# Optimization experiments

Measured on AMD Instinct MI355X. Metric: run time of the kernel, lower is better.

## Reference

```python
import jax, jax.numpy as jnp
import numpy as np

SIZE = 384  # output resolution
SCALE = (0.8, 1.0)


def _bilinear_crop_resize(img, cs, top, left):
    """img: [C,H,W]; cs/top/left: int32 scalars. Crop [top:top+cs, left:left+cs],
    resize to SIZE x SIZE with bilinear, align_corners=False (PyTorch semantics)."""
    csf = cs.astype(jnp.float32)
    # source coords within the crop, clamped like PyTorch (src = max(src,0), upper bounded)
    coords = (jnp.arange(SIZE, dtype=jnp.float32) + 0.5) * (csf / SIZE) - 0.5
    coords = jnp.clip(coords, 0.0, csf - 1.0)
    i0 = jnp.floor(coords).astype(jnp.int32)
    i1 = jnp.minimum(i0 + 1, cs - 1)
    w = coords - i0.astype(jnp.float32)  # [SIZE]
    y0, y1 = i0 + top, i1 + top
    x0, x1 = i0 + left, i1 + left
    wy, wx = w[:, None], w[None, :]
    g = lambda yy, xx: img[:, yy[:, None], xx[None, :]]  # [C,SIZE,SIZE]
    return (g(y0, x0) * (1 - wy) * (1 - wx)
            + g(y0, x1) * (1 - wy) * wx
            + g(y1, x0) * wy * (1 - wx)
            + g(y1, x1) * wy * wx)


def _nearest_crop_resize(msk, cs, top, left):
    """msk: [1,H,W]. PyTorch mode='nearest': src_idx = floor(dst * in/out)."""
    idx = jnp.floor(jnp.arange(SIZE, dtype=jnp.float32) * cs.astype(jnp.float32) / SIZE).astype(jnp.int32)
    idx = jnp.minimum(idx, cs - 1)
    y, x = idx + top, idx + left
    return msk[:, y[:, None], x[None, :]]


def setup_inputs() -> dict:
    key = jax.random.key(0)
    k1, k2, k3, k4, k5 = jax.random.split(key, 5)
    B, C, H, W = 32, 3, 512, 512
    image = jax.random.normal(k1, (B, C, H, W), dtype=jnp.float32)
    mask = (jax.random.uniform(k2, (B, 1, H, W)) > 0.5).astype(jnp.float32)
    scale = jax.random.uniform(k3, (B,), minval=SCALE[0], maxval=SCALE[1])
    crop_size = (scale * min(H, W)).astype(jnp.int32)
    max_y = (H - crop_size).astype(jnp.float32)
    max_x = (W - crop_size).astype(jnp.float32)
    top = jnp.where(max_y > 0, jnp.floor(jax.random.uniform(k4, (B,)) * max_y), 0.0).astype(jnp.int32)
    left = jnp.where(max_x > 0, jnp.floor(jax.random.uniform(k5, (B,)) * max_x), 0.0).astype(jnp.int32)
    return {"image": image, "mask": mask, "crop_size": crop_size, "top": top, "left": left}


def reference(image, mask, crop_size, top, left):
    img_out = jax.vmap(_bilinear_crop_resize)(image, crop_size, top, left)
    msk_out = jax.vmap(_nearest_crop_resize)(mask, crop_size, top, left)
    return img_out, msk_out
```

## Files before the change

### kernel.cpp

```cpp
#include <hip/hip_runtime.h>


constexpr int OUT = 384;
constexpr int H = 512;
constexpr int W = 512;
constexpr int B = 32;
constexpr int C = 3;
constexpr int RPB = 4;
constexpr int GPB = OUT / RPB;
constexpr int NBLK = B * GPB;
constexpr int BPX  = NBLK / 8;
constexpr int NSLOT = 6;
constexpr int LROWS = C * NSLOT;
constexpr int BUFSZ = LROWS * W;

typedef float f32x4 __attribute__((ext_vector_type(4)));

__global__ __launch_bounds__(OUT) void rrc_pair_kernel(
    const float* __restrict__ image,
    const float* __restrict__ mask,
    const int* __restrict__ crop_size,
    const int* __restrict__ top,
    const int* __restrict__ left,
    float* __restrict__ img_out,
    float* __restrict__ msk_out)
{
    __shared__ float lds[BUFSZ + 8];

    const int hw = blockIdx.x;
    const int logical = (hw & 7) * BPX + (hw >> 3);
    const int b  = logical / GPB;
    const int i0 = (logical % GPB) * RPB;
    const int tid = (int)threadIdx.x;

    const int cs = crop_size[b];
    const int t  = top[b];
    const int l  = left[b];
    const float csf = (float)cs;
    const float s   = csf / (float)OUT;

    float cy0 = ((float)i0 + 0.5f) * s - 0.5f;
    cy0 = fminf(fmaxf(cy0, 0.0f), csf - 1.0f);
    const int base_y = (int)floorf(cy0);

    const float* imgb = image + (size_t)b * C * H * W;

    #pragma unroll
    for (int k = 0; k < 6; ++k) {
        const int q   = tid + k * OUT;
        const int r   = q >> 7;
        const int col = (q & 127) * 4;
        const int c    = r / NSLOT;
        const int slot = r % NSLOT;
        const int y = min(t + base_y + slot, H - 1);
        const float* src = imgb + ((size_t)c * H + (size_t)y) * W + col;
        __builtin_amdgcn_global_load_lds(
            (const __attribute__((address_space(1))) void*)src,
            (__attribute__((address_space(3))) void*)&lds[q * 4],
            16, 0, 0);
    }
    if (tid < 8) lds[BUFSZ + tid] = 0.0f;

    float cx = ((float)tid + 0.5f) * s - 0.5f;
    cx = fminf(fmaxf(cx, 0.0f), csf - 1.0f);
    const int   ix0 = (int)floorf(cx);
    const float wx  = cx - (float)ix0;
    const int   x0  = ix0 + l;

    const int mx = min((tid * cs) / OUT, cs - 1) + l;

    float mval[RPB];
    #pragma unroll
    for (int r4 = 0; r4 < RPB; ++r4) {
        const int i = i0 + r4;
        int my = min((i * cs) / OUT, cs - 1);
        mval[r4] = mask[((size_t)b * H + (size_t)(my + t)) * W + mx];
    }

    __syncthreads();

    #pragma unroll
    for (int r4 = 0; r4 < RPB; ++r4) {
        const int i = i0 + r4;
        float cy = ((float)i + 0.5f) * s - 0.5f;
        cy = fminf(fmaxf(cy, 0.0f), csf - 1.0f);
        int   iy0 = (int)floorf(cy);
        int   iy1 = min(iy0 + 1, cs - 1);
        float wy  = cy - (float)iy0;
        const int slot0 = iy0 - base_y;
        const int slot1 = min(iy1 - base_y, NSLOT - 1);

        const float w00 = (1.0f - wy) * (1.0f - wx);
        const float w01 = (1.0f - wy) * wx;
        const float w10 = wy * (1.0f - wx);
        const float w11 = wy * wx;

        const size_t o_base = (size_t)b * C * OUT * OUT + (size_t)i * OUT + (size_t)tid;

        #pragma unroll
        for (int c = 0; c < C; ++c) {
            const float* rA = &lds[(c * NSLOT + slot0) * W + x0];
            const float* rB = &lds[(c * NSLOT + slot1) * W + x0];
            float v00 = rA[0], v01 = rA[1];
            float v10 = rB[0], v11 = rB[1];
            float rr = v00 * w00 + v01 * w01 + v10 * w10 + v11 * w11;
            __builtin_nontemporal_store(rr, img_out + o_base + (size_t)c * OUT * OUT);
        }
        __builtin_nontemporal_store(mval[r4],
            msk_out + (size_t)b * OUT * OUT + (size_t)i * OUT + (size_t)tid);
    }
}

extern "C" void kernel_launch(void* const* d_in, const int* in_sizes, int n_in,
                              void* d_out, int out_size, void* d_ws, size_t ws_size,
                              hipStream_t stream) {
    const float* image = (const float*)d_in[0];
    const float* mask  = (const float*)d_in[1];
    const int* cs      = (const int*)d_in[2];
    const int* top     = (const int*)d_in[3];
    const int* left    = (const int*)d_in[4];

    float* img_out = (float*)d_out;
    float* msk_out = img_out + (size_t)B * C * OUT * OUT;

    dim3 block(OUT);
    dim3 grid(NBLK);
    hipLaunchKernelGGL(rrc_pair_kernel, grid, block, 0, stream,
                       image, mask, cs, top, left, img_out, msk_out);
}
```

Baseline: 33.14 us.

## Split output rows into column stripes and stage only needed source columns in LDS

Each block now handles a 128-wide column stripe of 4 output rows instead of full 384-wide rows, so the grid is three times larger with 128-thread blocks. Only a 176-float-wide window of each source row, aligned to 4 floats, is loaded into LDS rather than the full 512-float row. This cuts wasted global loads of columns the block never reads and lowers LDS per block, which allows more blocks per CU. In exchange, blocks are smaller, per-block setup is repeated more often, and neighbouring stripes load overlapping columns.

```diff
diff --git a/kernel.cpp b/kernel.cpp
--- a/kernel.cpp
+++ b/kernel.cpp
@@ -8,15 +8,19 @@
 constexpr int C = 3;
 constexpr int RPB = 4;
 constexpr int GPB = OUT / RPB;
-constexpr int NBLK = B * GPB;
-constexpr int BPX  = NBLK / 8;
+constexpr int SW  = 128;
+constexpr int NSTRIPE = OUT / SW;
 constexpr int NSLOT = 6;
 constexpr int LROWS = C * NSLOT;
-constexpr int BUFSZ = LROWS * W;
+constexpr int NW  = 176;
+constexpr int NCH = NW / 4;
+constexpr int TOT_CHUNK = LROWS * NCH;
+constexpr int NBLK = B * GPB * NSTRIPE;
+constexpr int BPX  = NBLK / 8;
 
 typedef float f32x4 __attribute__((ext_vector_type(4)));
 
-__global__ __launch_bounds__(OUT) void rrc_pair_kernel(
+__global__ __launch_bounds__(128, 6) void rrc_pair_kernel(
     const float* __restrict__ image,
     const float* __restrict__ mask,
     const int* __restrict__ crop_size,
@@ -25,13 +29,18 @@
     float* __restrict__ img_out,
     float* __restrict__ msk_out)
 {
-    __shared__ float lds[BUFSZ + 8];
+    __shared__ float lds[LROWS * NW + 8];
 
     const int hw = blockIdx.x;
     const int logical = (hw & 7) * BPX + (hw >> 3);
-    const int b  = logical / GPB;
-    const int i0 = (logical % GPB) * RPB;
+    const int b   = logical / (GPB * NSTRIPE);
+    const int rem = logical % (GPB * NSTRIPE);
+    const int grp = rem / NSTRIPE;
+    const int st  = rem % NSTRIPE;
+    const int i0  = grp * RPB;
+    const int c0  = st * SW;
     const int tid = (int)threadIdx.x;
+    const int j   = c0 + tid;
 
     const int cs = crop_size[b];
     const int t  = top[b];
@@ -43,37 +52,43 @@
     cy0 = fminf(fmaxf(cy0, 0.0f), csf - 1.0f);
     const int base_y = (int)floorf(cy0);
 
+    float cx0 = ((float)c0 + 0.5f) * s - 0.5f;
+    cx0 = fminf(fmaxf(cx0, 0.0f), csf - 1.0f);
+    const int gx0 = (int)floorf(cx0);
+    const int cbg = min(l + gx0, W - NW) & ~3;
+
     const float* imgb = image + (size_t)b * C * H * W;
 
     #pragma unroll
-    for (int k = 0; k < 6; ++k) {
-        const int q   = tid + k * OUT;
-        const int r   = q >> 7;
-        const int col = (q & 127) * 4;
-        const int c    = r / NSLOT;
-        const int slot = r % NSLOT;
-        const int y = min(t + base_y + slot, H - 1);
-        const float* src = imgb + ((size_t)c * H + (size_t)y) * W + col;
-        __builtin_amdgcn_global_load_lds(
-            (const __attribute__((address_space(1))) void*)src,
-            (__attribute__((address_space(3))) void*)&lds[q * 4],
-            16, 0, 0);
+    for (int rd = 0; rd < 7; ++rd) {
+        const int q = rd * 128 + tid;
+        if (q < TOT_CHUNK) {
+            const int r   = q / NCH;
+            const int col = (q - r * NCH) * 4;
+            const int c    = r / NSLOT;
+            const int slot = r - c * NSLOT;
+            const int y = min(t + base_y + slot, H - 1);
+            const float* src = imgb + ((size_t)(c * H + y)) * W + cbg + col;
+            __builtin_amdgcn_global_load_lds(
+                (const __attribute__((address_space(1))) void*)src,
+                (__attribute__((address_space(3))) void*)&lds[q * 4],
+                16, 0, 0);
+        }
     }
-    if (tid < 8) lds[BUFSZ + tid] = 0.0f;
+    if (tid < 8) lds[LROWS * NW + tid] = 0.0f;
 
-    float cx = ((float)tid + 0.5f) * s - 0.5f;
+    float cx = ((float)j + 0.5f) * s - 0.5f;
     cx = fminf(fmaxf(cx, 0.0f), csf - 1.0f);
     const int   ix0 = (int)floorf(cx);
     const float wx  = cx - (float)ix0;
-    const int   x0  = ix0 + l;
+    const int   xoff = l + ix0 - cbg;
 
-    const int mx = min((tid * cs) / OUT, cs - 1) + l;
+    const int mx = min((j * cs) / OUT, cs - 1) + l;
 
     float mval[RPB];
     #pragma unroll
     for (int r4 = 0; r4 < RPB; ++r4) {
-        const int i = i0 + r4;
-        int my = min((i * cs) / OUT, cs - 1);
+        int my = min(((i0 + r4) * cs) / OUT, cs - 1);
         mval[r4] = mask[((size_t)b * H + (size_t)(my + t)) * W + mx];
     }
 
@@ -95,19 +110,19 @@
         const float w10 = wy * (1.0f - wx);
         const float w11 = wy * wx;
 
-        const size_t o_base = (size_t)b * C * OUT * OUT + (size_t)i * OUT + (size_t)tid;
+        const size_t o_base = (size_t)b * C * OUT * OUT + (size_t)i * OUT + (size_t)j;
 
         #pragma unroll
         for (int c = 0; c < C; ++c) {
-            const float* rA = &lds[(c * NSLOT + slot0) * W + x0];
-            const float* rB = &lds[(c * NSLOT + slot1) * W + x0];
+            const float* rA = &lds[(c * NSLOT + slot0) * NW + xoff];
+            const float* rB = &lds[(c * NSLOT + slot1) * NW + xoff];
             float v00 = rA[0], v01 = rA[1];
             float v10 = rB[0], v11 = rB[1];
             float rr = v00 * w00 + v01 * w01 + v10 * w10 + v11 * w11;
             __builtin_nontemporal_store(rr, img_out + o_base + (size_t)c * OUT * OUT);
         }
         __builtin_nontemporal_store(mval[r4],
-            msk_out + (size_t)b * OUT * OUT + (size_t)i * OUT + (size_t)tid);
+            msk_out + (size_t)b * OUT * OUT + (size_t)i * OUT + (size_t)j);
     }
 }
 
@@ -123,7 +138,7 @@
     float* img_out = (float*)d_out;
     float* msk_out = img_out + (size_t)B * C * OUT * OUT;
 
-    dim3 block(OUT);
+    dim3 block(128);
     dim3 grid(NBLK);
     hipLaunchKernelGGL(rrc_pair_kernel, grid, block, 0, stream,
                        image, mask, cs, top, left, img_out, msk_out);
```

Measured after the change: 31.79 us. 4.1% less time.
